# Kernel optimization log

Measured on AMD Instinct MI355X. Metric: run time of the kernel, lower is better.

The kernel has to match this reference:

```python
import jax, jax.numpy as jnp
import numpy as np

N = 20000       # nodes per graph
E = 320000      # edges per graph (avg degree 16)
R = 8           # num_relations
B = 2           # batch of graphs
DIMS = [128, 256, 256, 128]  # in -> hidden -> hidden -> out
SLOPE = 0.2     # LeakyReLU negative slope


def setup_inputs() -> dict:
    key = jax.random.key(0)
    ks = jax.random.split(key, 12)
    inp = {
        "x": jax.random.normal(ks[0], (B, N, DIMS[0]), dtype=jnp.float32),
        "edge_index": jax.random.randint(ks[1], (B, 2, E), 0, N, dtype=jnp.int32),
        "edge_type": jax.random.randint(ks[2], (B, E), 0, R, dtype=jnp.int32),
    }
    for l in range(3):
        cin, cout = DIMS[l], DIMS[l + 1]
        s = 1.0 / np.sqrt(cin)
        inp[f"W{l}"] = jax.random.normal(ks[3 + 3 * l], (R, cin, cout), jnp.float32) * s
        inp[f"root{l}"] = jax.random.normal(ks[4 + 3 * l], (cin, cout), jnp.float32) * s
        inp[f"b{l}"] = jnp.zeros((cout,), jnp.float32)
    return inp


def _rgcn_layer(h, src, dst, etype, W, root, b):
    """One RGCNConv (per-relation mean aggregation) on a single graph.
    h: (N,Cin), src/dst/etype: (E,), W: (R,Cin,Cout), root: (Cin,Cout), b: (Cout,)
    """
    # transform every node by every relation weight once: (N,R,Cout)
    h_rel = jnp.einsum('nc,rcd->nrd', h, W)
    # per-edge message: gather source node transformed by that edge's relation
    msg = h_rel[src, etype]                               # (E,Cout)
    # per-(target-node, relation) mean, as in PyG's per-relation propagate
    seg = dst * R + etype                                 # (E,)
    sums = jax.ops.segment_sum(msg, seg, num_segments=N * R)
    cnt = jax.ops.segment_sum(jnp.ones((msg.shape[0],), h.dtype), seg,
                              num_segments=N * R)
    mean = sums / jnp.maximum(cnt, 1.0)[:, None]          # (N*R,Cout)
    agg = mean.reshape(N, R, -1).sum(axis=1)              # (N,Cout)
    return agg + h @ root + b


def reference(x, edge_index, edge_type, W0, root0, b0, W1, root1, b1, W2, root2, b2):
    params = [(W0, root0, b0), (W1, root1, b1), (W2, root2, b2)]

    def single(xg, ei, et):
        src, dst = ei[0], ei[1]
        h = xg
        for (W, root, b) in params:
            h = _rgcn_layer(h, src, dst, et, W, root, b)
            h = jnp.where(h > 0, h, SLOPE * h)  # LeakyReLU(0.2); dropout=identity (eval)
        return h

    return jax.vmap(single)(x, edge_index, edge_type)
```

## Files before the change

kernel.cpp:

```cpp
#include <hip/hip_runtime.h>
#include <hip/hip_bf16.h>

#define NN 20000
#define EE 320000
#define RR 8
#define NR (NN * RR)
#define NB 40
#define SCAP 640

typedef float f32x4 __attribute__((ext_vector_type(4)));
typedef short s16x8 __attribute__((ext_vector_type(8)));

__device__ __forceinline__ unsigned short f2bf(float f) {
  unsigned u = __builtin_bit_cast(unsigned, f);
  unsigned r = u + 0x7FFFu + ((u >> 16) & 1u);
  return (unsigned short)(r >> 16);
}
__device__ __forceinline__ float bf2f(unsigned short u) {
  return __builtin_bit_cast(float, (unsigned)u << 16);
}
__device__ __forceinline__ void gload_lds16(const void* g, void* l) {
  __builtin_amdgcn_global_load_lds(
      (const __attribute__((address_space(1))) unsigned*)g,
      (__attribute__((address_space(3))) unsigned*)l, 16, 0, 0);
}

__global__ void k_count(const int* __restrict__ ei, const int* __restrict__ et,
                        int* __restrict__ cnt) {
  int e = blockIdx.x * blockDim.x + threadIdx.x;
  int g = e >= EE;
  int el = e - g * EE;
  int d = ei[(size_t)g * 2 * EE + EE + el];
  int t = et[(size_t)g * EE + el];
  atomicAdd(&cnt[(size_t)g * NR + d * RR + t], 1);
}

__global__ __launch_bounds__(1024) void k_scan1(const int* __restrict__ cnt,
                                                int* __restrict__ off,
                                                int* __restrict__ btot) {
  int g = blockIdx.y, b = blockIdx.x;
  const int* c = cnt + (size_t)g * NR;
  int* o = off + (size_t)g * NR;
  __shared__ int wsum[16];
  int lane = threadIdx.x & 63, w = threadIdx.x >> 6;
  int i = b * 4096 + (int)threadIdx.x * 4;
  int4 v = {0, 0, 0, 0};
  if (i + 3 < NR) v = *(const int4*)&c[i];
  else {
    if (i < NR) v.x = c[i];
    if (i + 1 < NR) v.y = c[i + 1];
    if (i + 2 < NR) v.z = c[i + 2];
  }
  int s0 = v.x, s1 = s0 + v.y, s2 = s1 + v.z, s3 = s2 + v.w;
  int s = s3;
  for (int d = 1; d < 64; d <<= 1) {
    int t = __shfl_up(s, d);
    if (lane >= d) s += t;
  }
  if (lane == 63) wsum[w] = s;
  __syncthreads();
  if (threadIdx.x < 16) {
    int ws = wsum[threadIdx.x];
    for (int d = 1; d < 16; d <<= 1) {
      int t = __shfl_up(ws, d);
      if ((int)threadIdx.x >= d) ws += t;
    }
    wsum[threadIdx.x] = ws;
  }
  __syncthreads();
  int excl = (w > 0 ? wsum[w - 1] : 0) + (s - s3);
  if (i < NR) o[i] = excl;
  if (i + 1 < NR) o[i + 1] = excl + s0;
  if (i + 2 < NR) o[i + 2] = excl + s1;
  if (i + 3 < NR) o[i + 3] = excl + s2;
  if (threadIdx.x == 0) btot[g * NB + b] = wsum[15];
}

__global__ void k_scan2(const int* __restrict__ btot, int* __restrict__ bof) {
  int g = threadIdx.x >> 6, lane = threadIdx.x & 63;
  int v = (lane < NB) ? btot[g * NB + lane] : 0;
  int s = v;
  for (int d = 1; d < 64; d <<= 1) {
    int t = __shfl_up(s, d);
    if (lane >= d) s += t;
  }
  if (lane < NB) bof[g * NB + lane] = s - v;
}

__global__ __launch_bounds__(1024) void k_scan3(int* __restrict__ off,
                                                const int* __restrict__ bof) {
  int g = blockIdx.y;
  int add = bof[g * NB + blockIdx.x];
  int i = blockIdx.x * 4096 + (int)threadIdx.x * 4;
  int* o = off + (size_t)g * NR;
  if (i + 3 < NR) {
    int4 v = *(const int4*)&o[i];
    v.x += add; v.y += add; v.z += add; v.w += add;
    *(int4*)&o[i] = v;
  } else {
    for (int j = i; j < NR; ++j) o[j] += add;
  }
}

__global__ void k_scatter(const int* __restrict__ ei, const int* __restrict__ et,
                          int* __restrict__ off, int* __restrict__ ssrc) {
  int e = blockIdx.x * blockDim.x + threadIdx.x;
  int g = e >= EE;
  int el = e - g * EE;
  int s = ei[(size_t)g * 2 * EE + el];
  int d = ei[(size_t)g * 2 * EE + EE + el];
  int t = et[(size_t)g * EE + el];
  int pos = atomicAdd(&off[(size_t)g * NR + d * RR + t], 1);
  ssrc[(size_t)g * EE + pos] = s;
}

__global__ void k_cvt(const float* __restrict__ x, unsigned short* __restrict__ hX) {
  int i = (blockIdx.x * blockDim.x + threadIdx.x) * 4;
  if (i >= 2 * NN * 128) return;
  int g = i >= NN * 128;
  int il = i - g * NN * 128;
  float4 v = *(const float4*)&x[i];
  ushort4 o;
  o.x = f2bf(v.x); o.y = f2bf(v.y); o.z = f2bf(v.z); o.w = f2bf(v.w);
  *(ushort4*)&hX[(size_t)g * NN * 256 + il] = o;
}

__global__ void k_btf(const float* __restrict__ W, const float* __restrict__ root,
                      unsigned short* __restrict__ btf, int Cin, int Cout,
                      int Ktot) {
  int idx = blockIdx.x * blockDim.x + threadIdx.x;
  if (idx >= Cout * Ktot) return;
  int j = idx & 7;
  int lane = (idx >> 3) & 63;
  int kk = (idx >> 9) & 1;
  int t = idx >> 10;
  int fr = t % (Cout / 16);
  int s = t / (Cout / 16);
  int co = fr * 16 + (lane & 15);
  int k = s * 64 + kk * 32 + (lane >> 4) * 8 + j;
  int r = k / Cin, ci = k - r * Cin;
  float v = (r < RR) ? W[((size_t)r * Cin + ci) * Cout + co]
                     : root[(size_t)ci * Cout + co];
  btf[idx] = f2bf(v);
}

#define LOADB(bb, s)                                                           \
  _Pragma("unroll") for (int kk = 0; kk < 2; ++kk)                             \
      _Pragma("unroll") for (int f = 0; f < 4; ++f) bb[kk][f] =                \
          *(const s16x8*)(btl +                                                \
                          (size_t)(((s) * (COUT / 16) + wn16 + f) * 2 + kk) *  \
                              512);

#define COPYB()                                                                \
  _Pragma("unroll") for (int kk = 0; kk < 2; ++kk)                             \
      _Pragma("unroll") for (int f = 0; f < 4; ++f) bc[kk][f] = bn[kk][f];

#define MFMA_STEP_C(c, bb)                                                     \
  do {                                                                         \
    _Pragma("unroll") for (int kk = 0; kk < 2; ++kk) {                         \
      s16x8 a[MF];                                                             \
      _Pragma("unroll") for (int f = 0; f < MF; ++f) {                         \
        int row = wm + f * 16 + (lane & 15);                                   \
        int colb = kk * 64 + (lane >> 4) * 16;                                 \
        a[f] = *(const s16x8*)(As + (c)*ASTR + row * 128 +                     \
                               (colb ^ ((row & 7) << 4)));                     \
      }                                                                        \
      _Pragma("unroll") for (int fm = 0; fm < MF; ++fm)                        \
          _Pragma("unroll") for (int fn = 0; fn < 4; ++fn)                     \
              acc[fm][fn] = __builtin_amdgcn_mfma_f32_16x16x32_bf16(           \
                  a[fm], bb[kk][fn], acc[fm][fn], 0, 0, 0);                    \
    }                                                                          \
  } while (0)

template <int CIN, int COUT, bool OUTF32>
__global__ __launch_bounds__(256) void k_fused(
    const int* __restrict__ ssrc, const int* __restrict__ off,
    const unsigned short* __restrict__ h, const unsigned short* __restrict__ btf,
    const float* __restrict__ bias, void* __restrict__ outp) {
  constexpr int KTOT = (RR + 1) * CIN;
  constexpr int NS = KTOT / 64;
  constexpr int CH = CIN / 64;
  constexpr int CPT = CIN / 8;
  constexpr int NCH = CPT / 8;
  constexpr int NWN = COUT / 64;
  constexpr int MW = 4 / NWN;
  constexpr int WR = 32 / MW;
  constexpr int MF = WR / 16;
  constexpr int ASTR = 4112;
  __shared__ char As[CH * ASTR];
  __shared__ int offs[32][9];
  __shared__ int sseg[SCAP];
  const int tid = threadIdx.x, lane = tid & 63, wave = tid >> 6;
  const int wn = (wave % NWN) * 64;
  const int wn16 = wn >> 4;
  const int wm = (wave / NWN) * WR;
  const int m0 = blockIdx.x * 32;
  const int g = blockIdx.z;
  ssrc += (size_t)g * EE;
  off += (size_t)g * NR;
  h += (size_t)g * NN * 256;

  for (int idx = tid; idx < 32 * 9; idx += 256) {
    int row = idx / 9, j = idx - row * 9;
    int seg0 = (m0 + row) * RR;
    offs[row][j] = (j == 0) ? (seg0 == 0 ? 0 : off[seg0 - 1]) : off[seg0 + j - 1];
  }
  const int segA = m0 * RR;
  const int ebase = (segA == 0) ? 0 : off[segA - 1];
  const int eend = off[(m0 + 32) * RR - 1];
  const int cntE = eend - ebase;
  const bool inl = cntE <= SCAP;
  if (inl)
    for (int i = tid; i < cntE; i += 256) sseg[i] = ssrc[ebase + i];
  __syncthreads();

  f32x4 acc[MF][4] = {};
  const int arow = tid >> 3;
  const int q = tid & 7;
  const int swzA = (arow & 7) << 4;
  const unsigned short* hq = h + q * CPT;
  const unsigned short* btl = btf + lane * 8;

  s16x8 bc[2][4], bn[2][4];
  LOADB(bc, 0);

  for (int r = 0; r <= RR; ++r) {
    s16x8 mb[NCH];
    if (r < RR) {
      float fa[NCH][8];
#pragma unroll
      for (int c = 0; c < NCH; ++c)
#pragma unroll
        for (int j = 0; j < 8; ++j) fa[c][j] = 0.f;
      int o0 = offs[arow][r], o1 = offs[arow][r + 1];
      int e = o0;
      for (; e + 1 < o1; e += 2) {
        int sa = inl ? sseg[e - ebase] : ssrc[e];
        int sb = inl ? sseg[e + 1 - ebase] : ssrc[e + 1];
        const unsigned short* pa = hq + (size_t)sa * CIN;
        const unsigned short* pb = hq + (size_t)sb * CIN;
#pragma unroll
        for (int c = 0; c < NCH; ++c) {
          s16x8 va = *(const s16x8*)(pa + c * 8);
          s16x8 vb = *(const s16x8*)(pb + c * 8);
#pragma unroll
          for (int j = 0; j < 8; ++j)
            fa[c][j] += bf2f((unsigned short)va[j]) + bf2f((unsigned short)vb[j]);
        }
      }
      if (e < o1) {
        int sa = inl ? sseg[e - ebase] : ssrc[e];
        const unsigned short* pa = hq + (size_t)sa * CIN;
#pragma unroll
        for (int c = 0; c < NCH; ++c) {
          s16x8 va = *(const s16x8*)(pa + c * 8);
#pragma unroll
          for (int j = 0; j < 8; ++j) fa[c][j] += bf2f((unsigned short)va[j]);
        }
      }
      float inv = 1.0f / fmaxf((float)(o1 - o0), 1.0f);
#pragma unroll
      for (int c = 0; c < NCH; ++c)
#pragma unroll
        for (int j = 0; j < 8; ++j) mb[c][j] = (short)f2bf(fa[c][j] * inv);
    }
    __syncthreads();
    if (r < RR) {
#pragma unroll
      for (int ch = 0; ch < NCH; ++ch) {
        int colb = (q * CPT + ch * 8) * 2;
        int ct = colb >> 7;
        int wb = colb & 127;
        *(s16x8*)(As + ct * ASTR + arow * 128 + (wb ^ swzA)) = mb[ch];
      }
    } else {
#pragma unroll
      for (int i = 0; i < CH; ++i) {
        int o = i * ASTR + wave * 1024;
        int ob = wave * 1024 + lane * 16;
        int row = (ob >> 7) & 31;
        int wb = ob & 127;
        gload_lds16((const char*)h + ((size_t)(m0 + row) * CIN + i * 64) * 2 +
                        (wb ^ ((row & 7) << 4)),
                    As + o);
      }
    }
    __syncthreads();
#pragma unroll
    for (int c = 0; c < CH; ++c) {
      int s = r * CH + c;
      if (s + 1 < NS) { LOADB(bn, s + 1); }
      MFMA_STEP_C(c, bc);
      if (s + 1 < NS) { COPYB(); }
    }
  }
#pragma unroll
  for (int fm = 0; fm < MF; ++fm) {
    int rbase = m0 + wm + fm * 16 + (lane >> 4) * 4;
#pragma unroll
    for (int fn = 0; fn < 4; ++fn) {
      int col = wn + fn * 16 + (lane & 15);
      float bv = bias[col];
#pragma unroll
      for (int v = 0; v < 4; ++v) {
        int row = rbase + v;
        float xv = acc[fm][fn][v] + bv;
        xv = xv > 0.f ? xv : 0.2f * xv;
        if constexpr (OUTF32)
          ((float*)outp)[(size_t)g * NN * COUT + (size_t)row * COUT + col] = xv;
        else
          ((unsigned short*)outp)[(size_t)g * NN * 256 + (size_t)row * COUT +
                                  col] = f2bf(xv);
      }
    }
  }
}

extern "C" void kernel_launch(void* const* d_in, const int* in_sizes, int n_in,
                              void* d_out, int out_size, void* d_ws, size_t ws_size,
                              hipStream_t stream) {
  const float* x  = (const float*)d_in[0];
  const int* ei   = (const int*)d_in[1];
  const int* etp  = (const int*)d_in[2];
  const float* W0 = (const float*)d_in[3];
  const float* r0 = (const float*)d_in[4];
  const float* b0 = (const float*)d_in[5];
  const float* W1 = (const float*)d_in[6];
  const float* r1 = (const float*)d_in[7];
  const float* b1 = (const float*)d_in[8];
  const float* W2 = (const float*)d_in[9];
  const float* r2 = (const float*)d_in[10];
  const float* b2 = (const float*)d_in[11];

  char* p = (char*)d_ws;
  unsigned short* hX  = (unsigned short*)p; p += (size_t)2 * NN * 256 * 2;
  unsigned short* h_a = (unsigned short*)p; p += (size_t)2 * NN * 256 * 2;
  int* cnt  = (int*)p; p += (size_t)2 * NR * 4;
  int* off  = (int*)p; p += (size_t)2 * NR * 4;
  int* btot = (int*)p; p += (size_t)2 * NB * 4;
  int* bof  = (int*)p; p += (size_t)2 * NB * 4;
  int* ssrc = (int*)p; p += (size_t)2 * EE * 4;
  unsigned short* bt0 = (unsigned short*)p; p += (size_t)256 * 1152 * 2;
  unsigned short* bt1 = (unsigned short*)p; p += (size_t)256 * 2304 * 2;
  unsigned short* bt2 = (unsigned short*)p; p += (size_t)128 * 2304 * 2;

  k_btf<<<(256 * 1152 + 255) / 256, 256, 0, stream>>>(W0, r0, bt0, 128, 256, 1152);
  k_btf<<<(256 * 2304 + 255) / 256, 256, 0, stream>>>(W1, r1, bt1, 256, 256, 2304);
  k_btf<<<(128 * 2304 + 255) / 256, 256, 0, stream>>>(W2, r2, bt2, 256, 128, 2304);

  (void)hipMemsetAsync(cnt, 0, (size_t)2 * NR * 4, stream);
  k_count<<<2 * EE / 256, 256, 0, stream>>>(ei, etp, cnt);
  k_scan1<<<dim3(NB, 2), 1024, 0, stream>>>(cnt, off, btot);
  k_scan2<<<1, 128, 0, stream>>>(btot, bof);
  k_scan3<<<dim3(NB, 2), 1024, 0, stream>>>(off, bof);
  k_cvt<<<2 * NN * 128 / 4 / 256, 256, 0, stream>>>(x, hX);
  k_scatter<<<2 * EE / 256, 256, 0, stream>>>(ei, etp, off, ssrc);

  k_fused<128, 256, false><<<dim3(625, 1, 2), 256, 0, stream>>>(
      ssrc, off, hX, bt0, b0, h_a);
  k_fused<256, 256, false><<<dim3(625, 1, 2), 256, 0, stream>>>(
      ssrc, off, h_a, bt1, b1, hX);
  k_fused<256, 128, true><<<dim3(625, 1, 2), 256, 0, stream>>>(
      ssrc, off, hX, bt2, b2, d_out);
}
```

Baseline: 420.3 us.

## Double-buffer LDS A tiles to overlap gather-mean with MFMA and unpack bf16 via masks

Splits the A-tile LDS buffer into two halves so the gather/mean of relation r+1 is written into one buffer while MFMAs consume relation r from the other. This drops one of the two barriers per relation step. It also replaces per-element bf16-to-float conversion with 32-bit mask/shift unpacking of packed pairs. The cost is doubled LDS use per block, which can lower occupancy, and the overlap depends on the compiler interleaving the global gathers with the MFMAs.

```diff
diff --git a/kernel.cpp b/kernel.cpp
--- a/kernel.cpp
+++ b/kernel.cpp
@@ -155,14 +155,14 @@
   _Pragma("unroll") for (int kk = 0; kk < 2; ++kk)                             \
       _Pragma("unroll") for (int f = 0; f < 4; ++f) bc[kk][f] = bn[kk][f];
 
-#define MFMA_STEP_C(c, bb)                                                     \
+#define MFMA_STEP_C(Ab, c, bb)                                                 \
   do {                                                                         \
     _Pragma("unroll") for (int kk = 0; kk < 2; ++kk) {                         \
       s16x8 a[MF];                                                             \
       _Pragma("unroll") for (int f = 0; f < MF; ++f) {                         \
         int row = wm + f * 16 + (lane & 15);                                   \
         int colb = kk * 64 + (lane >> 4) * 16;                                 \
-        a[f] = *(const s16x8*)(As + (c)*ASTR + row * 128 +                     \
+        a[f] = *(const s16x8*)((Ab) + (c)*ASTR + row * 128 +                   \
                                (colb ^ ((row & 7) << 4)));                     \
       }                                                                        \
       _Pragma("unroll") for (int fm = 0; fm < MF; ++fm)                        \
@@ -171,6 +171,18 @@
                   a[fm], bb[kk][fn], acc[fm][fn], 0, 0, 0);                    \
     }                                                                          \
   } while (0)
+
+#define ACC4(u)                                                                \
+  {                                                                            \
+    faH[c][0] += __builtin_bit_cast(float, (u).x & 0xFFFF0000u);               \
+    faL[c][0] += __builtin_bit_cast(float, (u).x << 16);                       \
+    faH[c][1] += __builtin_bit_cast(float, (u).y & 0xFFFF0000u);               \
+    faL[c][1] += __builtin_bit_cast(float, (u).y << 16);                       \
+    faH[c][2] += __builtin_bit_cast(float, (u).z & 0xFFFF0000u);               \
+    faL[c][2] += __builtin_bit_cast(float, (u).z << 16);                       \
+    faH[c][3] += __builtin_bit_cast(float, (u).w & 0xFFFF0000u);               \
+    faL[c][3] += __builtin_bit_cast(float, (u).w << 16);                       \
+  }
 
 template <int CIN, int COUT, bool OUTF32>
 __global__ __launch_bounds__(256) void k_fused(
@@ -187,7 +199,7 @@
   constexpr int WR = 32 / MW;
   constexpr int MF = WR / 16;
   constexpr int ASTR = 4112;
-  __shared__ char As[CH * ASTR];
+  __shared__ char As[2][CH * ASTR];
   __shared__ int offs[32][9];
   __shared__ int sseg[SCAP];
   const int tid = threadIdx.x, lane = tid & 63, wave = tid >> 6;
@@ -221,79 +233,84 @@
   const unsigned short* hq = h + q * CPT;
   const unsigned short* btl = btf + lane * 8;
 
+  auto produce = [&](int r, int buf) {
+    float faL[NCH][4], faH[NCH][4];
+#pragma unroll
+    for (int c = 0; c < NCH; ++c)
+#pragma unroll
+      for (int w = 0; w < 4; ++w) { faL[c][w] = 0.f; faH[c][w] = 0.f; }
+    int o0 = offs[arow][r], o1 = offs[arow][r + 1];
+    int e = o0;
+    for (; e + 1 < o1; e += 2) {
+      int sa = inl ? sseg[e - ebase] : ssrc[e];
+      int sb = inl ? sseg[e + 1 - ebase] : ssrc[e + 1];
+      const unsigned short* pa = hq + (size_t)sa * CIN;
+      const unsigned short* pb = hq + (size_t)sb * CIN;
+#pragma unroll
+      for (int c = 0; c < NCH; ++c) {
+        uint4 ua = *(const uint4*)(pa + c * 8);
+        uint4 ub = *(const uint4*)(pb + c * 8);
+        ACC4(ua);
+        ACC4(ub);
+      }
+    }
+    if (e < o1) {
+      int sa = inl ? sseg[e - ebase] : ssrc[e];
+      const unsigned short* pa = hq + (size_t)sa * CIN;
+#pragma unroll
+      for (int c = 0; c < NCH; ++c) {
+        uint4 ua = *(const uint4*)(pa + c * 8);
+        ACC4(ua);
+      }
+    }
+    float inv = 1.0f / fmaxf((float)(o1 - o0), 1.0f);
+#pragma unroll
+    for (int c = 0; c < NCH; ++c) {
+      s16x8 mbv;
+#pragma unroll
+      for (int w = 0; w < 4; ++w) {
+        mbv[2 * w] = (short)f2bf(faL[c][w] * inv);
+        mbv[2 * w + 1] = (short)f2bf(faH[c][w] * inv);
+      }
+      int colb = (q * CPT + c * 8) * 2;
+      int ct = colb >> 7;
+      int wb = colb & 127;
+      *(s16x8*)(As[buf] + ct * ASTR + arow * 128 + (wb ^ swzA)) = mbv;
+    }
+  };
+
+  auto root_stage = [&]() {
+#pragma unroll
+    for (int i = 0; i < CH; ++i) {
+      int o = i * ASTR + wave * 1024;
+      int ob = wave * 1024 + lane * 16;
+      int row = (ob >> 7) & 31;
+      int wb = ob & 127;
+      gload_lds16((const char*)h + ((size_t)(m0 + row) * CIN + i * 64) * 2 +
+                      (wb ^ ((row & 7) << 4)),
+                  As[RR & 1] + o);
+    }
+  };
+
   s16x8 bc[2][4], bn[2][4];
   LOADB(bc, 0);
+  produce(0, 0);
+  __syncthreads();
 
   for (int r = 0; r <= RR; ++r) {
-    s16x8 mb[NCH];
-    if (r < RR) {
-      float fa[NCH][8];
-#pragma unroll
-      for (int c = 0; c < NCH; ++c)
-#pragma unroll
-        for (int j = 0; j < 8; ++j) fa[c][j] = 0.f;
-      int o0 = offs[arow][r], o1 = offs[arow][r + 1];
-      int e = o0;
-      for (; e + 1 < o1; e += 2) {
-        int sa = inl ? sseg[e - ebase] : ssrc[e];
-        int sb = inl ? sseg[e + 1 - ebase] : ssrc[e + 1];
-        const unsigned short* pa = hq + (size_t)sa * CIN;
-        const unsigned short* pb = hq + (size_t)sb * CIN;
-#pragma unroll
-        for (int c = 0; c < NCH; ++c) {
-          s16x8 va = *(const s16x8*)(pa + c * 8);
-          s16x8 vb = *(const s16x8*)(pb + c * 8);
-#pragma unroll
-          for (int j = 0; j < 8; ++j)
-            fa[c][j] += bf2f((unsigned short)va[j]) + bf2f((unsigned short)vb[j]);
-        }
-      }
-      if (e < o1) {
-        int sa = inl ? sseg[e - ebase] : ssrc[e];
-        const unsigned short* pa = hq + (size_t)sa * CIN;
-#pragma unroll
-        for (int c = 0; c < NCH; ++c) {
-          s16x8 va = *(const s16x8*)(pa + c * 8);
-#pragma unroll
-          for (int j = 0; j < 8; ++j) fa[c][j] += bf2f((unsigned short)va[j]);
-        }
-      }
-      float inv = 1.0f / fmaxf((float)(o1 - o0), 1.0f);
-#pragma unroll
-      for (int c = 0; c < NCH; ++c)
-#pragma unroll
-        for (int j = 0; j < 8; ++j) mb[c][j] = (short)f2bf(fa[c][j] * inv);
-    }
-    __syncthreads();
-    if (r < RR) {
-#pragma unroll
-      for (int ch = 0; ch < NCH; ++ch) {
-        int colb = (q * CPT + ch * 8) * 2;
-        int ct = colb >> 7;
-        int wb = colb & 127;
-        *(s16x8*)(As + ct * ASTR + arow * 128 + (wb ^ swzA)) = mb[ch];
-      }
-    } else {
-#pragma unroll
-      for (int i = 0; i < CH; ++i) {
-        int o = i * ASTR + wave * 1024;
-        int ob = wave * 1024 + lane * 16;
-        int row = (ob >> 7) & 31;
-        int wb = ob & 127;
-        gload_lds16((const char*)h + ((size_t)(m0 + row) * CIN + i * 64) * 2 +
-                        (wb ^ ((row & 7) << 4)),
-                    As + o);
-      }
-    }
-    __syncthreads();
+    const char* Ab = As[r & 1];
 #pragma unroll
     for (int c = 0; c < CH; ++c) {
       int s = r * CH + c;
       if (s + 1 < NS) { LOADB(bn, s + 1); }
-      MFMA_STEP_C(c, bc);
+      MFMA_STEP_C(Ab, c, bc);
       if (s + 1 < NS) { COPYB(); }
     }
-  }
+    if (r + 1 < RR) produce(r + 1, (r + 1) & 1);
+    else if (r + 1 == RR) root_stage();
+    __syncthreads();
+  }
+
 #pragma unroll
   for (int fm = 0; fm < MF; ++fm) {
     int rbase = m0 + wm + fm * 16 + (lane >> 4) * 4;
```

Measured after the change: 387.4 us. 7.8% less time.
